# Kernel tuning notes

Hardware: AMD Instinct MI355X
Metric: run time of the kernel (lower is better)

## Reference

```python
import math
import jax, jax.numpy as jnp
import numpy as np
from jax import lax

B = 32; SEQ_LEN = 1024; PRED_LEN = 1024; ENC_IN = 7; MARK = 4; C_OUT = 7
D_MODEL = 128; D_INNER = 256; D_STATE = 16; D_CONV = 4; DT_RANK = 8; N_LAYER = 2


def setup_inputs() -> dict:
    key = jax.random.key(0)
    ks = jax.random.split(key, 16)
    f32 = jnp.float32
    inp = {}
    inp['x_enc'] = jax.random.normal(ks[0], (B, SEQ_LEN, ENC_IN), f32)
    inp['x_mark_enc'] = jax.random.uniform(ks[1], (B, SEQ_LEN, MARK), f32) - 0.5
    inp['x_dec'] = jax.random.normal(ks[2], (B, 512, ENC_IN), f32)
    inp['x_mark_dec'] = jax.random.uniform(ks[3], (B, 512, MARK), f32) - 0.5
    inp['token_W'] = jax.random.normal(ks[4], (D_MODEL, ENC_IN, 3), f32) * (1.0 / math.sqrt(3 * ENC_IN))
    inp['temporal_W'] = jax.random.normal(ks[5], (D_MODEL, MARK), f32) * 0.1
    inp['norm_w'] = jnp.ones((N_LAYER, D_MODEL), f32)
    inp['norm_b'] = jnp.zeros((N_LAYER, D_MODEL), f32)
    inp['in_proj_W'] = jax.random.normal(ks[6], (N_LAYER, 2 * D_INNER, D_MODEL), f32) * (1.0 / math.sqrt(D_MODEL))
    inp['conv_W'] = jax.random.normal(ks[7], (N_LAYER, D_INNER, D_CONV), f32) * 0.3
    inp['conv_b'] = jnp.zeros((N_LAYER, D_INNER), f32)
    inp['x_proj_W'] = jax.random.normal(ks[8], (N_LAYER, DT_RANK + 2 * D_STATE, D_INNER), f32) * (1.0 / math.sqrt(D_INNER))
    inp['dt_proj_W'] = jax.random.normal(ks[9], (N_LAYER, D_INNER, DT_RANK), f32) * (1.0 / math.sqrt(DT_RANK))
    inp['dt_proj_b'] = jax.random.normal(ks[10], (N_LAYER, D_INNER), f32) * 0.5 - 4.0  # softplus -> small dt, like mamba init
    inp['A_log'] = jnp.log(jnp.broadcast_to(jnp.arange(1, D_STATE + 1, dtype=f32), (N_LAYER, D_INNER, D_STATE)))
    inp['D_param'] = jnp.ones((N_LAYER, D_INNER), f32)
    inp['out_proj_W'] = jax.random.normal(ks[11], (N_LAYER, D_MODEL, D_INNER), f32) * (1.0 / math.sqrt(D_INNER))
    inp['normf_w'] = jnp.ones((D_MODEL,), f32)
    inp['normf_b'] = jnp.zeros((D_MODEL,), f32)
    inp['out_W'] = jax.random.normal(ks[12], (C_OUT, D_MODEL), f32) * (1.0 / math.sqrt(D_MODEL))
    return inp


def _layer_norm(x, w, b):
    mu = x.mean(-1, keepdims=True)
    var = ((x - mu) ** 2).mean(-1, keepdims=True)
    return (x - mu) * lax.rsqrt(var + 1e-5) * w + b


def _silu(x):
    return x * jax.nn.sigmoid(x)


def _pos_embedding(L, d):
    pos = jnp.arange(L, dtype=jnp.float32)[:, None]
    div = jnp.exp(jnp.arange(0, d, 2, dtype=jnp.float32) * (-math.log(10000.0) / d))
    pe = jnp.zeros((L, d), jnp.float32)
    pe = pe.at[:, 0::2].set(jnp.sin(pos * div))
    pe = pe.at[:, 1::2].set(jnp.cos(pos * div))
    return pe


def _embed(x_enc, x_mark_enc, token_W, temporal_W):
    # TokenEmbedding: Conv1d(enc_in->d_model, k=3, circular padding, no bias)
    xp = jnp.concatenate([x_enc[:, -1:], x_enc, x_enc[:, :1]], axis=1)  # circular pad by 1
    val = lax.conv_general_dilated(xp, token_W.transpose(2, 1, 0), (1,), 'VALID',
                                   dimension_numbers=('NWC', 'WIO', 'NWC'))
    temp = jnp.einsum('blf,df->bld', x_mark_enc, temporal_W)  # TimeFeatureEmbedding (no bias)
    return val + temp + _pos_embedding(x_enc.shape[1], D_MODEL)


def _mamba_mixer(x, in_W, cW, cb, xp_W, dtW, dtb, A_log_l, D_l, o_W):
    Bb, L, _ = x.shape
    xz = jnp.einsum('bld,ed->ble', x, in_W)  # [B,L,2*d_inner]
    xi, z = jnp.split(xz, 2, axis=-1)
    # causal depthwise conv1d (kernel d_conv)
    xpad = jnp.pad(xi, ((0, 0), (D_CONV - 1, 0), (0, 0)))
    kern = cW.T[:, None, :]  # [d_conv, 1, d_inner]
    u = lax.conv_general_dilated(xpad, kern, (1,), 'VALID', dimension_numbers=('NWC', 'WIO', 'NWC'),
                                 feature_group_count=D_INNER) + cb
    u = _silu(u)
    dbc = jnp.einsum('bld,ed->ble', u, xp_W)
    dt_r = dbc[..., :DT_RANK]
    Bm = dbc[..., DT_RANK:DT_RANK + D_STATE]
    Cm = dbc[..., DT_RANK + D_STATE:]
    dt = jax.nn.softplus(jnp.einsum('blr,dr->bld', dt_r, dtW) + dtb)  # [B,L,d_inner]
    A = -jnp.exp(A_log_l)  # [d_inner, d_state]

    def step(h, inp):
        dt_t, B_t, C_t, u_t = inp  # [B,d_inner], [B,d_state], [B,d_state], [B,d_inner]
        dA = jnp.exp(dt_t[..., None] * A)
        h = dA * h + dt_t[..., None] * B_t[:, None, :] * u_t[..., None]
        y = jnp.einsum('bds,bs->bd', h, C_t)
        return h, y

    h0 = jnp.zeros((Bb, D_INNER, D_STATE), x.dtype)
    _, ys = lax.scan(step, h0, (dt.transpose(1, 0, 2), Bm.transpose(1, 0, 2),
                                Cm.transpose(1, 0, 2), u.transpose(1, 0, 2)))
    y = ys.transpose(1, 0, 2) + u * D_l  # skip connection D*u
    y = y * _silu(z)
    return jnp.einsum('ble,de->bld', y, o_W)


def _mixer_model(x, norm_w, norm_b, in_proj_W, conv_W, conv_b, x_proj_W, dt_proj_W, dt_proj_b,
                 A_log, D_param, out_proj_W, normf_w, normf_b):
    hidden, residual = x, None
    for l in range(N_LAYER):
        residual = hidden if residual is None else hidden + residual
        hidden = _mamba_mixer(_layer_norm(residual, norm_w[l], norm_b[l]), in_proj_W[l], conv_W[l],
                              conv_b[l], x_proj_W[l], dt_proj_W[l], dt_proj_b[l], A_log[l],
                              D_param[l], out_proj_W[l])
    return _layer_norm(hidden + residual, normf_w, normf_b)


def reference(x_enc, x_mark_enc, x_dec, x_mark_dec, token_W, temporal_W, norm_w, norm_b,
              in_proj_W, conv_W, conv_b, x_proj_W, dt_proj_W, dt_proj_b, A_log, D_param,
              out_proj_W, normf_w, normf_b, out_W):
    h = _embed(x_enc, x_mark_enc, token_W, temporal_W)
    outs = []
    for _ in range((PRED_LEN - 1) // SEQ_LEN + 1):
        h = _mixer_model(h, norm_w, norm_b, in_proj_W, conv_W, conv_b, x_proj_W, dt_proj_W,
                         dt_proj_b, A_log, D_param, out_proj_W, normf_w, normf_b)
        outs.append(h)
    mamba_out = jnp.concatenate(outs, axis=1)[:, :PRED_LEN]
    return jnp.einsum('bld,cd->blc', mamba_out, out_W)
```

## Files before the change

kernel.cpp:

```cpp
#include <hip/hip_runtime.h>
#include <math.h>

#define B_  32
#define L_  1024
#define M_  (B_*L_)
#define DM  128
#define DI  256
#define DS  16
#define DC  4
#define DR  8
#define NL  2

typedef unsigned int  uint32;
typedef unsigned short ush;
typedef __attribute__((ext_vector_type(8))) short bf16x8;
typedef __attribute__((ext_vector_type(4))) float f32x4;

__device__ __forceinline__ float silu_f(float x) { return x / (1.f + expf(-x)); }
__device__ __forceinline__ float softplus_f(float x) {
    return fmaxf(x, 0.f) + log1pf(expf(-fabsf(x)));
}
__device__ __forceinline__ ush f2bf(float x) {
    union { float f; uint32 u; } v; v.f = x;
    uint32 lsb = (v.u >> 16) & 1u;
    v.u += 0x7fffu + lsb;
    return (ush)(v.u >> 16);
}
__device__ __forceinline__ void split2(float x, ush& h, ush& l) {
    h = f2bf(x);
    float fh = __uint_as_float(((uint32)h) << 16);
    l = f2bf(x - fh);
}
__device__ __forceinline__ uint32 pack_pair(float x) {
    ush h, l; split2(x, h, l);
    return (uint32)h | ((uint32)l << 16);
}
__device__ __forceinline__ float unpack_pair(uint32 v) {
    return __uint_as_float(v << 16) + __uint_as_float(v & 0xffff0000u);
}

__global__ __launch_bounds__(256) void cvt_pair_kernel(
        const float* __restrict__ src, ush* __restrict__ h, ush* __restrict__ l, int n) {
    int i = blockIdx.x * 256 + threadIdx.x;
    if (i < n) { ush hh, ll; split2(src[i], hh, ll); h[i] = hh; l[i] = ll; }
}

__global__ __launch_bounds__(256) void pe_kernel(float* __restrict__ pe) {
    int idx = blockIdx.x * 256 + threadIdx.x;
    int t = idx >> 6, i = idx & 63;
    float div = expf(-0.07195578415606394f * (float)(2 * i));
    float ang = (float)t * div;
    pe[t * 128 + 2 * i]     = sinf(ang);
    pe[t * 128 + 2 * i + 1] = cosf(ang);
}

__global__ __launch_bounds__(256) void embed_kernel(
        const float* __restrict__ x_enc, const float* __restrict__ x_mark,
        const float* __restrict__ tokW, const float* __restrict__ tempW,
        const float* __restrict__ pe, float* __restrict__ out) {
    int idx = blockIdx.x * 256 + threadIdx.x;
    int d = idx & 127;
    int m = idx >> 7;
    int b = m >> 10, t = m & 1023;
    const float* xb = x_enc + (size_t)b * L_ * 7;
    float acc = pe[t * 128 + d];
    #pragma unroll
    for (int w = 0; w < 3; ++w) {
        int tt = t + w - 1;
        tt = (tt < 0) ? (L_ - 1) : (tt >= L_ ? 0 : tt);
        const float* xr = xb + tt * 7;
        #pragma unroll
        for (int f = 0; f < 7; ++f) acc += xr[f] * tokW[(d * 7 + f) * 3 + w];
    }
    const float* mr = x_mark + (size_t)m * 4;
    #pragma unroll
    for (int f = 0; f < 4; ++f) acc += mr[f] * tempW[d * 4 + f];
    out[idx] = acc;
}

__global__ __launch_bounds__(256) void ln_kernel(
        const float* __restrict__ a, const float* __restrict__ b,
        const float* __restrict__ w, const float* __restrict__ bias,
        float* __restrict__ out_f32, ush* __restrict__ outh, ush* __restrict__ outl,
        float* __restrict__ out_res) {
    int wv = threadIdx.x >> 6, lane = threadIdx.x & 63;
    size_t m = (size_t)blockIdx.x * 4 + wv;
    size_t base = m * DM;
    float x0 = a[base + lane], x1 = a[base + lane + 64];
    if (b) { x0 += b[base + lane]; x1 += b[base + lane + 64]; }
    if (out_res) { out_res[base + lane] = x0; out_res[base + lane + 64] = x1; }
    float s = x0 + x1;
    #pragma unroll
    for (int o = 1; o < 64; o <<= 1) s += __shfl_xor(s, o, 64);
    float mu = s * (1.f / 128.f);
    float d0 = x0 - mu, d1 = x1 - mu;
    float v = d0 * d0 + d1 * d1;
    #pragma unroll
    for (int o = 1; o < 64; o <<= 1) v += __shfl_xor(v, o, 64);
    float inv = rsqrtf(v * (1.f / 128.f) + 1e-5f);
    float r0 = d0 * inv * w[lane]      + bias[lane];
    float r1 = d1 * inv * w[lane + 64] + bias[lane + 64];
    if (out_f32) {
        out_f32[base + lane] = r0; out_f32[base + lane + 64] = r1;
    } else {
        ush h, l;
        split2(r0, h, l); outh[base + lane] = h;      outl[base + lane] = l;
        split2(r1, h, l); outh[base + lane + 64] = h; outl[base + lane + 64] = l;
    }
}

__global__ __launch_bounds__(256) void gemm_inproj_mfma(
        const ush* __restrict__ Ah, const ush* __restrict__ Al,
        const ush* __restrict__ Wh, const ush* __restrict__ Wl,
        float* __restrict__ xiT, float* __restrict__ zsilT) {
    int bm = blockIdx.y * 128, bn = blockIdx.x * 128;
    int w = threadIdx.x >> 6, l = threadIdx.x & 63;
    int lm = l & 15, lk8 = (l >> 4) * 8;
    f32x4 acc[2][8];
    #pragma unroll
    for (int mi = 0; mi < 2; ++mi)
        #pragma unroll
        for (int ni = 0; ni < 8; ++ni) acc[mi][ni] = {0.f, 0.f, 0.f, 0.f};
    const ush* ah = Ah + (size_t)(bm + w * 32 + lm) * 128;
    const ush* al = Al + (size_t)(bm + w * 32 + lm) * 128;
    const ush* wh = Wh + (size_t)(bn + lm) * 128;
    const ush* wl = Wl + (size_t)(bn + lm) * 128;
    for (int k0 = 0; k0 < 128; k0 += 32) {
        bf16x8 aH[2], aL[2];
        #pragma unroll
        for (int mi = 0; mi < 2; ++mi) {
            aH[mi] = *(const bf16x8*)(ah + mi * 16 * 128 + k0 + lk8);
            aL[mi] = *(const bf16x8*)(al + mi * 16 * 128 + k0 + lk8);
        }
        #pragma unroll
        for (int ni = 0; ni < 8; ++ni) {
            bf16x8 wH = *(const bf16x8*)(wh + ni * 16 * 128 + k0 + lk8);
            bf16x8 wLo = *(const bf16x8*)(wl + ni * 16 * 128 + k0 + lk8);
            #pragma unroll
            for (int mi = 0; mi < 2; ++mi) {
                acc[mi][ni] = __builtin_amdgcn_mfma_f32_16x16x32_bf16(aL[mi], wH,  acc[mi][ni], 0, 0, 0);
                acc[mi][ni] = __builtin_amdgcn_mfma_f32_16x16x32_bf16(aH[mi], wLo, acc[mi][ni], 0, 0, 0);
                acc[mi][ni] = __builtin_amdgcn_mfma_f32_16x16x32_bf16(aH[mi], wH,  acc[mi][ni], 0, 0, 0);
            }
        }
    }
    int b = bm >> 10;
    int tl0 = (bm & 1023) + w * 32 + (l >> 4) * 4;
    #pragma unroll
    for (int ni = 0; ni < 8; ++ni) {
        int n = bn + ni * 16 + lm;
        #pragma unroll
        for (int mi = 0; mi < 2; ++mi) {
            int tl = tl0 + mi * 16;
            f32x4 v = acc[mi][ni];
            if (bn < 256) {
                *(f32x4*)(xiT + ((size_t)(b * 256 + n)) * 1024 + tl) = v;
            } else {
                f32x4 r;
                #pragma unroll
                for (int i = 0; i < 4; ++i) r[i] = silu_f(v[i]);
                *(f32x4*)(zsilT + ((size_t)(b * 256 + n - 256)) * 1024 + tl) = r;
            }
        }
    }
}

template<int NF, int KTOT>
__global__ __launch_bounds__(256) void gemm_at_mfma(
        const uint32* __restrict__ A32, const ush* __restrict__ Wh,
        const ush* __restrict__ Wl, int Nvalid,
        float* __restrict__ Cnm, float* __restrict__ Cmn) {
    __shared__ uint32 As[128][68];
    int bm = blockIdx.x * 128;
    int b = bm >> 10, tloc = bm & 1023;
    int tid = threadIdx.x;
    int w = tid >> 6, l = tid & 63;
    int lm = l & 15, lk8 = (l >> 4) * 8;
    f32x4 acc[2][NF];
    #pragma unroll
    for (int mi = 0; mi < 2; ++mi)
        #pragma unroll
        for (int ni = 0; ni < NF; ++ni) acc[mi][ni] = {0.f, 0.f, 0.f, 0.f};

    for (int k0 = 0; k0 < KTOT; k0 += 64) {
        __syncthreads();
        {
            int k = tid >> 2, mq = tid & 3;
            const uint32* src = A32 + ((size_t)(b * KTOT + k0 + k)) * 1024 + tloc + mq * 32;
            #pragma unroll
            for (int c = 0; c < 8; ++c) {
                uint4 v = *(const uint4*)(src + c * 4);
                As[mq * 32 + c * 4 + 0][k] = v.x;
                As[mq * 32 + c * 4 + 1][k] = v.y;
                As[mq * 32 + c * 4 + 2][k] = v.z;
                As[mq * 32 + c * 4 + 3][k] = v.w;
            }
        }
        __syncthreads();
        #pragma unroll
        for (int ks = 0; ks < 2; ++ks) {
            int kk = ks * 32 + lk8;
            bf16x8 aH[2], aL[2];
            #pragma unroll
            for (int mi = 0; mi < 2; ++mi) {
                int m = w * 32 + mi * 16 + lm;
                uint4 p0 = *(const uint4*)&As[m][kk];
                uint4 p1 = *(const uint4*)&As[m][kk + 4];
                uint32 u[8] = {p0.x, p0.y, p0.z, p0.w, p1.x, p1.y, p1.z, p1.w};
                bf16x8 h, lo;
                #pragma unroll
                for (int j = 0; j < 8; ++j) {
                    h[j]  = (short)(u[j] & 0xffffu);
                    lo[j] = (short)(u[j] >> 16);
                }
                aH[mi] = h; aL[mi] = lo;
            }
            #pragma unroll
            for (int ni = 0; ni < NF; ++ni) {
                int n = ni * 16 + lm;
                bf16x8 wH = {0,0,0,0,0,0,0,0}, wLo = {0,0,0,0,0,0,0,0};
                if (n < Nvalid) {
                    wH  = *(const bf16x8*)(Wh + (size_t)n * KTOT + k0 + ks * 32 + lk8);
                    wLo = *(const bf16x8*)(Wl + (size_t)n * KTOT + k0 + ks * 32 + lk8);
                }
                #pragma unroll
                for (int mi = 0; mi < 2; ++mi) {
                    acc[mi][ni] = __builtin_amdgcn_mfma_f32_16x16x32_bf16(aL[mi], wH,  acc[mi][ni], 0, 0, 0);
                    acc[mi][ni] = __builtin_amdgcn_mfma_f32_16x16x32_bf16(aH[mi], wLo, acc[mi][ni], 0, 0, 0);
                    acc[mi][ni] = __builtin_amdgcn_mfma_f32_16x16x32_bf16(aH[mi], wH,  acc[mi][ni], 0, 0, 0);
                }
            }
        }
    }
    int m0 = w * 32 + (l >> 4) * 4;
    #pragma unroll
    for (int ni = 0; ni < NF; ++ni) {
        int n = ni * 16 + lm;
        #pragma unroll
        for (int mi = 0; mi < 2; ++mi) {
            f32x4 v = acc[mi][ni];
            int mg = bm + m0 + mi * 16;
            if (Cnm) {
                if (n < Nvalid) *(f32x4*)(Cnm + (size_t)n * M_ + mg) = v;
            } else {
                #pragma unroll
                for (int r = 0; r < 4; ++r)
                    Cmn[(size_t)(mg + r) * Nvalid + n] = v[r];
            }
        }
    }
}

__global__ __launch_bounds__(256) void conv_T_kernel(
        const float* __restrict__ xiT, const float* __restrict__ cw,
        const float* __restrict__ cb, uint32* __restrict__ uT32) {
    int wv = threadIdx.x >> 6, lane = threadIdx.x & 63;
    int rid = blockIdx.x * 4 + wv;
    int d = rid & 255;
    const float* src = xiT + (size_t)rid * 1024;
    int t0 = lane * 16;
    float x[20];
    {
        float4 p = (lane > 0) ? *(const float4*)(src + t0 - 4)
                              : make_float4(0.f, 0.f, 0.f, 0.f);
        *(float4*)&x[0] = p;
        #pragma unroll
        for (int c = 0; c < 4; ++c)
            *(float4*)&x[4 + c * 4] = *(const float4*)(src + t0 + c * 4);
    }
    float4 w4 = ((const float4*)cw)[d];
    float bias = cb[d];
    uint32* dst = uT32 + (size_t)rid * 1024 + t0;
    #pragma unroll
    for (int c = 0; c < 4; ++c) {
        uint4 o;
        uint32 ov[4];
        #pragma unroll
        for (int i = 0; i < 4; ++i) {
            int k = c * 4 + i;
            float acc = bias + x[k + 1] * w4.x + x[k + 2] * w4.y
                             + x[k + 3] * w4.z + x[k + 4] * w4.w;
            ov[i] = pack_pair(silu_f(acc));
        }
        o.x = ov[0]; o.y = ov[1]; o.z = ov[2]; o.w = ov[3];
        *(uint4*)(dst + c * 4) = o;
    }
}

__global__ __launch_bounds__(256) void dtT_kernel(
        const float* __restrict__ dbcT, const float* __restrict__ dtW,
        const float* __restrict__ dtb, float* __restrict__ dtT) {
    int n = threadIdx.x;
    int m0 = blockIdx.x * 64;
    int b = m0 >> 10, t0 = m0 & 1023;
    float wk[8];
    *(float4*)&wk[0] = ((const float4*)dtW)[n * 2];
    *(float4*)&wk[4] = ((const float4*)dtW)[n * 2 + 1];
    float bias = dtb[n];
    float* dst = dtT + ((size_t)(b * 256 + n)) * 1024 + t0;
    for (int r4 = 0; r4 < 64; r4 += 4) {
        float col[8][4];
        #pragma unroll
        for (int k = 0; k < 8; ++k)
            *(float4*)col[k] = *(const float4*)(dbcT + (size_t)k * M_ + m0 + r4);
        float o[4];
        #pragma unroll
        for (int i = 0; i < 4; ++i) {
            float a = bias;
            #pragma unroll
            for (int k = 0; k < 8; ++k) a += col[k][i] * wk[k];
            o[i] = softplus_f(a);
        }
        *(float4*)(dst + r4) = make_float4(o[0], o[1], o[2], o[3]);
    }
}

__global__ __launch_bounds__(256) void scan5_kernel(
        const float* __restrict__ dtT, const uint32* __restrict__ uT32,
        const float* __restrict__ dbcT, const float* __restrict__ A_log,
        const float* __restrict__ zsilT, const float* __restrict__ Dp,
        uint32* __restrict__ yT32) {
    int wv = threadIdx.x >> 6, lane = threadIdx.x & 63;
    int wid = blockIdx.x * 4 + wv;
    int b = wid >> 8, d = wid & 255;
    size_t base = (size_t)wid * 1024 + lane * 16;

    float dt[16], du[16], y[16], pcA[16], pcB[16];
    {
        const float4* p = (const float4*)(dtT + base);
        const uint4*  q = (const uint4*)(uT32 + base);
        #pragma unroll
        for (int c = 0; c < 4; ++c) {
            float4 dv = p[c]; uint4 uv = q[c];
            dt[c * 4 + 0] = dv.x; dt[c * 4 + 1] = dv.y; dt[c * 4 + 2] = dv.z; dt[c * 4 + 3] = dv.w;
            du[c * 4 + 0] = dv.x * unpack_pair(uv.x);
            du[c * 4 + 1] = dv.y * unpack_pair(uv.y);
            du[c * 4 + 2] = dv.z * unpack_pair(uv.z);
            du[c * 4 + 3] = dv.w * unpack_pair(uv.w);
        }
        #pragma unroll
        for (int i = 0; i < 16; ++i) y[i] = 0.f;
    }
    const float* Bb = dbcT + (size_t)8  * M_ + (size_t)b * 1024 + lane * 16;
    const float* Cb = dbcT + (size_t)24 * M_ + (size_t)b * 1024 + lane * 16;
    const float* Arow = A_log + d * 16;

    for (int p = 0; p < 8; ++p) {
        int s0 = 2 * p, s1 = 2 * p + 1;
        float4 B0[4], B1[4], C0[4], C1[4];
        #pragma unroll
        for (int c = 0; c < 4; ++c) {
            B0[c] = *(const float4*)(Bb + (size_t)s0 * M_ + c * 4);
            B1[c] = *(const float4*)(Bb + (size_t)s1 * M_ + c * 4);
            C0[c] = *(const float4*)(Cb + (size_t)s0 * M_ + c * 4);
            C1[c] = *(const float4*)(Cb + (size_t)s1 * M_ + c * 4);
        }
        float A2a = -expf(Arow[s0]) * 1.4426950408889634f;
        float A2b = -expf(Arow[s1]) * 1.4426950408889634f;
        float h0 = 0.f, P0 = 1.f, h1 = 0.f, P1 = 1.f;
        #pragma unroll
        for (int c = 0; c < 4; ++c) {
            float Bv0[4] = {B0[c].x, B0[c].y, B0[c].z, B0[c].w};
            float Cv0[4] = {C0[c].x, C0[c].y, C0[c].z, C0[c].w};
            float Bv1[4] = {B1[c].x, B1[c].y, B1[c].z, B1[c].w};
            float Cv1[4] = {C1[c].x, C1[c].y, C1[c].z, C1[c].w};
            #pragma unroll
            for (int i = 0; i < 4; ++i) {
                int ii = c * 4 + i;
                float a0 = __builtin_amdgcn_exp2f(dt[ii] * A2a);
                float a1 = __builtin_amdgcn_exp2f(dt[ii] * A2b);
                h0 = a0 * h0 + du[ii] * Bv0[i];  P0 *= a0;
                h1 = a1 * h1 + du[ii] * Bv1[i];  P1 *= a1;
                y[ii] += h0 * Cv0[i] + h1 * Cv1[i];
                pcA[ii] = P0 * Cv0[i];
                pcB[ii] = P1 * Cv1[i];
            }
        }
        float Aag0 = P0, E0 = h0, Aag1 = P1, E1 = h1;
        #pragma unroll
        for (int dlt = 1; dlt < 64; dlt <<= 1) {
            float Au0 = __shfl_up(Aag0, dlt, 64), Eu0 = __shfl_up(E0, dlt, 64);
            float Au1 = __shfl_up(Aag1, dlt, 64), Eu1 = __shfl_up(E1, dlt, 64);
            if (lane >= dlt) {
                E0 = Aag0 * Eu0 + E0;  Aag0 *= Au0;
                E1 = Aag1 * Eu1 + E1;  Aag1 *= Au1;
            }
        }
        float car0 = __shfl_up(E0, 1, 64), car1 = __shfl_up(E1, 1, 64);
        if (lane == 0) { car0 = 0.f; car1 = 0.f; }
        #pragma unroll
        for (int i = 0; i < 16; ++i) y[i] += car0 * pcA[i] + car1 * pcB[i];
    }

    float Dv = Dp[d];
    const float4* qz = (const float4*)(zsilT + base);
    uint32* dst = yT32 + base;
    #pragma unroll
    for (int c = 0; c < 4; ++c) {
        float4 zv = qz[c];
        float za[4] = {zv.x, zv.y, zv.z, zv.w};
        uint32 ov[4];
        #pragma unroll
        for (int i = 0; i < 4; ++i) {
            int ii = c * 4 + i;
            float u = (dt[ii] > 0.f) ? du[ii] * __builtin_amdgcn_rcpf(dt[ii]) : 0.f;
            ov[i] = pack_pair((y[ii] + u * Dv) * za[i]);
        }
        uint4 o; o.x = ov[0]; o.y = ov[1]; o.z = ov[2]; o.w = ov[3];
        *(uint4*)(dst + c * 4) = o;
    }
}

__global__ __launch_bounds__(256) void outproj_kernel(
        const float* __restrict__ x, const float* __restrict__ W,
        float* __restrict__ out) {
    int wv = threadIdx.x >> 6, lane = threadIdx.x & 63;
    size_t m = (size_t)blockIdx.x * 4 + wv;
    float x0 = x[m * 128 + lane], x1 = x[m * 128 + lane + 64];
    #pragma unroll
    for (int c = 0; c < 7; ++c) {
        float p = x0 * W[c * 128 + lane] + x1 * W[c * 128 + lane + 64];
        #pragma unroll
        for (int o = 1; o < 64; o <<= 1) p += __shfl_xor(p, o, 64);
        if (lane == 0) out[m * 7 + c] = p;
    }
}

extern "C" void kernel_launch(void* const* d_in, const int* in_sizes, int n_in,
                              void* d_out, int out_size, void* d_ws, size_t ws_size,
                              hipStream_t stream) {
    const float* x_enc  = (const float*)d_in[0];
    const float* x_mark = (const float*)d_in[1];
    const float* tokW   = (const float*)d_in[4];
    const float* tempW  = (const float*)d_in[5];
    const float* norm_w = (const float*)d_in[6];
    const float* norm_b = (const float*)d_in[7];
    const float* inW    = (const float*)d_in[8];
    const float* convW  = (const float*)d_in[9];
    const float* convB  = (const float*)d_in[10];
    const float* xpW    = (const float*)d_in[11];
    const float* dtW    = (const float*)d_in[12];
    const float* dtbp   = (const float*)d_in[13];
    const float* A_log  = (const float*)d_in[14];
    const float* Dp     = (const float*)d_in[15];
    const float* outW   = (const float*)d_in[16];
    const float* nfw    = (const float*)d_in[17];
    const float* nfb    = (const float*)d_in[18];
    const float* finW   = (const float*)d_in[19];
    float* out = (float*)d_out;

    float* ws = (float*)d_ws;
    size_t o = 0;
    float*  hidden   = ws + o; o += (size_t)M_ * DM;
    float*  residual = ws + o; o += (size_t)M_ * DM;
    float*  xlnF     = ws + o; o += (size_t)M_ * DM;
    float*  xiT      = ws + o; o += (size_t)M_ * DI;
    float*  zsilT    = ws + o; o += (size_t)M_ * DI;
    uint32* uT32     = (uint32*)(ws + o); o += (size_t)M_ * DI;
    float*  dbcT     = ws + o; o += (size_t)M_ * 40;
    float*  dtT      = ws + o; o += (size_t)M_ * DI;
    uint32* yT32     = (uint32*)(ws + o); o += (size_t)M_ * DI;
    ush* inWh  = (ush*)(ws + o); o += (size_t)NL * 512 * DM / 2;
    ush* inWl  = (ush*)(ws + o); o += (size_t)NL * 512 * DM / 2;
    ush* xpWh  = (ush*)(ws + o); o += (size_t)NL * 40 * DI / 2;
    ush* xpWl  = (ush*)(ws + o); o += (size_t)NL * 40 * DI / 2;
    ush* outWh = (ush*)(ws + o); o += (size_t)NL * DM * DI / 2;
    ush* outWl = (ush*)(ws + o); o += (size_t)NL * DM * DI / 2;
    ush* xlnh = (ush*)xlnF;
    ush* xlnl = xlnh + (size_t)M_ * DM;
    float* pe = dbcT;

    dim3 blk(256);
    pe_kernel<<<1024 * 64 / 256, blk, 0, stream>>>(pe);
    embed_kernel<<<M_ * DM / 256, blk, 0, stream>>>(x_enc, x_mark, tokW, tempW, pe, hidden);
    {
        int n1 = NL * 512 * DM, n2 = NL * 40 * DI, n3 = NL * DM * DI;
        cvt_pair_kernel<<<(n1 + 255) / 256, blk, 0, stream>>>(inW,  inWh,  inWl,  n1);
        cvt_pair_kernel<<<(n2 + 255) / 256, blk, 0, stream>>>(xpW,  xpWh,  xpWl,  n2);
        cvt_pair_kernel<<<(n3 + 255) / 256, blk, 0, stream>>>(outW, outWh, outWl, n3);
    }

    for (int l = 0; l < NL; ++l) {
        ln_kernel<<<M_ / 4, blk, 0, stream>>>(hidden, l ? residual : nullptr,
                                              norm_w + l * DM, norm_b + l * DM,
                                              nullptr, xlnh, xlnl, residual);
        gemm_inproj_mfma<<<dim3(4, M_ / 128), blk, 0, stream>>>(
            xlnh, xlnl, inWh + (size_t)l * 512 * DM, inWl + (size_t)l * 512 * DM,
            xiT, zsilT);
        conv_T_kernel<<<B_ * DI / 4, blk, 0, stream>>>(xiT, convW + l * DI * DC,
                                                       convB + l * DI, uT32);
        gemm_at_mfma<3, 256><<<M_ / 128, blk, 0, stream>>>(
            uT32, xpWh + (size_t)l * 40 * DI, xpWl + (size_t)l * 40 * DI,
            40, dbcT, nullptr);
        dtT_kernel<<<M_ / 64, blk, 0, stream>>>(dbcT, dtW + l * DI * DR,
                                                dtbp + l * DI, dtT);
        scan5_kernel<<<B_ * DI / 4, blk, 0, stream>>>(dtT, uT32, dbcT,
                                                      A_log + l * DI * DS, zsilT,
                                                      Dp + l * DI, yT32);
        gemm_at_mfma<8, 256><<<M_ / 128, blk, 0, stream>>>(
            yT32, outWh + (size_t)l * DM * DI, outWl + (size_t)l * DM * DI,
            128, nullptr, hidden);
    }

    ln_kernel<<<M_ / 4, blk, 0, stream>>>(hidden, residual, nfw, nfb,
                                          xlnF, nullptr, nullptr, nullptr);
    outproj_kernel<<<M_ / 4, blk, 0, stream>>>(xlnF, finW, out);
}
```

Measured before the change: 629.4 us.

## Fuse dt projection into scan kernel and final layernorm into output projection

The dt projection plus softplus is now computed inside the scan kernel from the dbc rows, so the separate dtT kernel and its M×256 float intermediate buffer are gone. The final layernorm is fused with the 7-channel output projection, which removes one full-size write and read of the normalized hidden state and one kernel launch. In exchange, the scan does extra loads of the 8 dt-rank rows and extra FMAs and softplus per element, repeated across the 256 channels of each batch.

```diff
diff --git a/kernel.cpp b/kernel.cpp
--- a/kernel.cpp
+++ b/kernel.cpp
@@ -81,14 +81,14 @@
 __global__ __launch_bounds__(256) void ln_kernel(
         const float* __restrict__ a, const float* __restrict__ b,
         const float* __restrict__ w, const float* __restrict__ bias,
-        float* __restrict__ out_f32, ush* __restrict__ outh, ush* __restrict__ outl,
+        ush* __restrict__ outh, ush* __restrict__ outl,
         float* __restrict__ out_res) {
     int wv = threadIdx.x >> 6, lane = threadIdx.x & 63;
     size_t m = (size_t)blockIdx.x * 4 + wv;
     size_t base = m * DM;
     float x0 = a[base + lane], x1 = a[base + lane + 64];
     if (b) { x0 += b[base + lane]; x1 += b[base + lane + 64]; }
-    if (out_res) { out_res[base + lane] = x0; out_res[base + lane + 64] = x1; }
+    out_res[base + lane] = x0; out_res[base + lane + 64] = x1;
     float s = x0 + x1;
     #pragma unroll
     for (int o = 1; o < 64; o <<= 1) s += __shfl_xor(s, o, 64);
@@ -100,12 +100,37 @@
     float inv = rsqrtf(v * (1.f / 128.f) + 1e-5f);
     float r0 = d0 * inv * w[lane]      + bias[lane];
     float r1 = d1 * inv * w[lane + 64] + bias[lane + 64];
-    if (out_f32) {
-        out_f32[base + lane] = r0; out_f32[base + lane + 64] = r1;
-    } else {
-        ush h, l;
-        split2(r0, h, l); outh[base + lane] = h;      outl[base + lane] = l;
-        split2(r1, h, l); outh[base + lane + 64] = h; outl[base + lane + 64] = l;
+    ush h, l;
+    split2(r0, h, l); outh[base + lane] = h;      outl[base + lane] = l;
+    split2(r1, h, l); outh[base + lane + 64] = h; outl[base + lane + 64] = l;
+}
+
+__global__ __launch_bounds__(256) void ln_out_kernel(
+        const float* __restrict__ a, const float* __restrict__ b,
+        const float* __restrict__ w, const float* __restrict__ bias,
+        const float* __restrict__ finW, float* __restrict__ out) {
+    int wv = threadIdx.x >> 6, lane = threadIdx.x & 63;
+    size_t m = (size_t)blockIdx.x * 4 + wv;
+    size_t base = m * DM;
+    float x0 = a[base + lane] + b[base + lane];
+    float x1 = a[base + lane + 64] + b[base + lane + 64];
+    float s = x0 + x1;
+    #pragma unroll
+    for (int o = 1; o < 64; o <<= 1) s += __shfl_xor(s, o, 64);
+    float mu = s * (1.f / 128.f);
+    float d0 = x0 - mu, d1 = x1 - mu;
+    float v = d0 * d0 + d1 * d1;
+    #pragma unroll
+    for (int o = 1; o < 64; o <<= 1) v += __shfl_xor(v, o, 64);
+    float inv = rsqrtf(v * (1.f / 128.f) + 1e-5f);
+    float r0 = d0 * inv * w[lane]      + bias[lane];
+    float r1 = d1 * inv * w[lane + 64] + bias[lane + 64];
+    #pragma unroll
+    for (int c = 0; c < 7; ++c) {
+        float p = r0 * finW[c * 128 + lane] + r1 * finW[c * 128 + lane + 64];
+        #pragma unroll
+        for (int o = 1; o < 64; o <<= 1) p += __shfl_xor(p, o, 64);
+        if (lane == 0) out[m * 7 + c] = p;
     }
 }
 
@@ -287,62 +312,48 @@
     }
 }
 
-__global__ __launch_bounds__(256) void dtT_kernel(
-        const float* __restrict__ dbcT, const float* __restrict__ dtW,
-        const float* __restrict__ dtb, float* __restrict__ dtT) {
-    int n = threadIdx.x;
-    int m0 = blockIdx.x * 64;
-    int b = m0 >> 10, t0 = m0 & 1023;
-    float wk[8];
-    *(float4*)&wk[0] = ((const float4*)dtW)[n * 2];
-    *(float4*)&wk[4] = ((const float4*)dtW)[n * 2 + 1];
-    float bias = dtb[n];
-    float* dst = dtT + ((size_t)(b * 256 + n)) * 1024 + t0;
-    for (int r4 = 0; r4 < 64; r4 += 4) {
-        float col[8][4];
-        #pragma unroll
-        for (int k = 0; k < 8; ++k)
-            *(float4*)col[k] = *(const float4*)(dbcT + (size_t)k * M_ + m0 + r4);
-        float o[4];
-        #pragma unroll
-        for (int i = 0; i < 4; ++i) {
-            float a = bias;
-            #pragma unroll
-            for (int k = 0; k < 8; ++k) a += col[k][i] * wk[k];
-            o[i] = softplus_f(a);
-        }
-        *(float4*)(dst + r4) = make_float4(o[0], o[1], o[2], o[3]);
-    }
-}
-
-__global__ __launch_bounds__(256) void scan5_kernel(
-        const float* __restrict__ dtT, const uint32* __restrict__ uT32,
-        const float* __restrict__ dbcT, const float* __restrict__ A_log,
-        const float* __restrict__ zsilT, const float* __restrict__ Dp,
-        uint32* __restrict__ yT32) {
+__global__ __launch_bounds__(256) void scan6_kernel(
+        const uint32* __restrict__ uT32, const float* __restrict__ dbcT,
+        const float* __restrict__ A_log, const float* __restrict__ zsilT,
+        const float* __restrict__ Dp, const float* __restrict__ dtW,
+        const float* __restrict__ dtb, uint32* __restrict__ yT32) {
     int wv = threadIdx.x >> 6, lane = threadIdx.x & 63;
     int wid = blockIdx.x * 4 + wv;
     int b = wid >> 8, d = wid & 255;
     size_t base = (size_t)wid * 1024 + lane * 16;
+    size_t m0 = (size_t)b * 1024 + lane * 16;
+
+    float wk[8];
+    *(float4*)&wk[0] = ((const float4*)dtW)[d * 2];
+    *(float4*)&wk[4] = ((const float4*)dtW)[d * 2 + 1];
+    float bias = dtb[d];
 
     float dt[16], du[16], y[16], pcA[16], pcB[16];
     {
-        const float4* p = (const float4*)(dtT + base);
-        const uint4*  q = (const uint4*)(uT32 + base);
+        const uint4* q = (const uint4*)(uT32 + base);
         #pragma unroll
         for (int c = 0; c < 4; ++c) {
-            float4 dv = p[c]; uint4 uv = q[c];
-            dt[c * 4 + 0] = dv.x; dt[c * 4 + 1] = dv.y; dt[c * 4 + 2] = dv.z; dt[c * 4 + 3] = dv.w;
-            du[c * 4 + 0] = dv.x * unpack_pair(uv.x);
-            du[c * 4 + 1] = dv.y * unpack_pair(uv.y);
-            du[c * 4 + 2] = dv.z * unpack_pair(uv.z);
-            du[c * 4 + 3] = dv.w * unpack_pair(uv.w);
+            float col[8][4];
+            #pragma unroll
+            for (int k = 0; k < 8; ++k)
+                *(float4*)col[k] = *(const float4*)(dbcT + (size_t)k * M_ + m0 + c * 4);
+            uint4 uv = q[c];
+            uint32 ua[4] = {uv.x, uv.y, uv.z, uv.w};
+            #pragma unroll
+            for (int i = 0; i < 4; ++i) {
+                float a = bias;
+                #pragma unroll
+                for (int k = 0; k < 8; ++k) a = fmaf(col[k][i], wk[k], a);
+                float dtv = softplus_f(a);
+                dt[c * 4 + i] = dtv;
+                du[c * 4 + i] = dtv * unpack_pair(ua[i]);
+            }
         }
         #pragma unroll
         for (int i = 0; i < 16; ++i) y[i] = 0.f;
     }
-    const float* Bb = dbcT + (size_t)8  * M_ + (size_t)b * 1024 + lane * 16;
-    const float* Cb = dbcT + (size_t)24 * M_ + (size_t)b * 1024 + lane * 16;
+    const float* Bb = dbcT + (size_t)8  * M_ + m0;
+    const float* Cb = dbcT + (size_t)24 * M_ + m0;
     const float* Arow = A_log + d * 16;
 
     for (int p = 0; p < 8; ++p) {
@@ -408,21 +419,6 @@
         }
         uint4 o; o.x = ov[0]; o.y = ov[1]; o.z = ov[2]; o.w = ov[3];
         *(uint4*)(dst + c * 4) = o;
-    }
-}
-
-__global__ __launch_bounds__(256) void outproj_kernel(
-        const float* __restrict__ x, const float* __restrict__ W,
-        float* __restrict__ out) {
-    int wv = threadIdx.x >> 6, lane = threadIdx.x & 63;
-    size_t m = (size_t)blockIdx.x * 4 + wv;
-    float x0 = x[m * 128 + lane], x1 = x[m * 128 + lane + 64];
-    #pragma unroll
-    for (int c = 0; c < 7; ++c) {
-        float p = x0 * W[c * 128 + lane] + x1 * W[c * 128 + lane + 64];
-        #pragma unroll
-        for (int o = 1; o < 64; o <<= 1) p += __shfl_xor(p, o, 64);
-        if (lane == 0) out[m * 7 + c] = p;
     }
 }
 
@@ -453,12 +449,11 @@
     size_t o = 0;
     float*  hidden   = ws + o; o += (size_t)M_ * DM;
     float*  residual = ws + o; o += (size_t)M_ * DM;
-    float*  xlnF     = ws + o; o += (size_t)M_ * DM;
+    float*  xlnP     = ws + o; o += (size_t)M_ * DM;
     float*  xiT      = ws + o; o += (size_t)M_ * DI;
     float*  zsilT    = ws + o; o += (size_t)M_ * DI;
     uint32* uT32     = (uint32*)(ws + o); o += (size_t)M_ * DI;
     float*  dbcT     = ws + o; o += (size_t)M_ * 40;
-    float*  dtT      = ws + o; o += (size_t)M_ * DI;
     uint32* yT32     = (uint32*)(ws + o); o += (size_t)M_ * DI;
     ush* inWh  = (ush*)(ws + o); o += (size_t)NL * 512 * DM / 2;
     ush* inWl  = (ush*)(ws + o); o += (size_t)NL * 512 * DM / 2;
@@ -466,7 +461,7 @@
     ush* xpWl  = (ush*)(ws + o); o += (size_t)NL * 40 * DI / 2;
     ush* outWh = (ush*)(ws + o); o += (size_t)NL * DM * DI / 2;
     ush* outWl = (ush*)(ws + o); o += (size_t)NL * DM * DI / 2;
-    ush* xlnh = (ush*)xlnF;
+    ush* xlnh = (ush*)xlnP;
     ush* xlnl = xlnh + (size_t)M_ * DM;
     float* pe = dbcT;
 
@@ -483,7 +478,7 @@
     for (int l = 0; l < NL; ++l) {
         ln_kernel<<<M_ / 4, blk, 0, stream>>>(hidden, l ? residual : nullptr,
                                               norm_w + l * DM, norm_b + l * DM,
-                                              nullptr, xlnh, xlnl, residual);
+                                              xlnh, xlnl, residual);
         gemm_inproj_mfma<<<dim3(4, M_ / 128), blk, 0, stream>>>(
             xlnh, xlnl, inWh + (size_t)l * 512 * DM, inWl + (size_t)l * 512 * DM,
             xiT, zsilT);
@@ -492,17 +487,15 @@
         gemm_at_mfma<3, 256><<<M_ / 128, blk, 0, stream>>>(
             uT32, xpWh + (size_t)l * 40 * DI, xpWl + (size_t)l * 40 * DI,
             40, dbcT, nullptr);
-        dtT_kernel<<<M_ / 64, blk, 0, stream>>>(dbcT, dtW + l * DI * DR,
-                                                dtbp + l * DI, dtT);
-        scan5_kernel<<<B_ * DI / 4, blk, 0, stream>>>(dtT, uT32, dbcT,
+        scan6_kernel<<<B_ * DI / 4, blk, 0, stream>>>(uT32, dbcT,
                                                       A_log + l * DI * DS, zsilT,
-                                                      Dp + l * DI, yT32);
+                                                      Dp + l * DI,
+                                                      dtW + (size_t)l * DI * DR,
+                                                      dtbp + l * DI, yT32);
         gemm_at_mfma<8, 256><<<M_ / 128, blk, 0, stream>>>(
             yT32, outWh + (size_t)l * DM * DI, outWl + (size_t)l * DM * DI,
             128, nullptr, hidden);
     }
 
-    ln_kernel<<<M_ / 4, blk, 0, stream>>>(hidden, residual, nfw, nfb,
-                                          xlnF, nullptr, nullptr, nullptr);
-    outproj_kernel<<<M_ / 4, blk, 0, stream>>>(xlnF, finW, out);
-}
+    ln_out_kernel<<<M_ / 4, blk, 0, stream>>>(hidden, residual, nfw, nfb, finW, out);
+}
```

Result: faster. 600.9 us (-4.5%).

## Split scan sequence across two waves, prefetch B/C, fuse final LN with output projection

Applied to the files above, without the earlier changes.

The selective scan now assigns each (batch, channel) sequence to two wavefronts, each handling 512 timesteps with 8 per lane. The first half's carry is passed through shared memory with a block barrier, which doubles the number of waves for better latency hiding and fewer registers per lane. B/C state loads are software-prefetched one state pair ahead, and the p loop is fully unrolled. Separately, the final layer norm is fused with the 7-channel output projection, which drops a full f32 intermediate write and read; the cost is an extra __syncthreads per state pair in the scan.

```diff
diff --git a/kernel.cpp b/kernel.cpp
--- a/kernel.cpp
+++ b/kernel.cpp
@@ -81,14 +81,14 @@
 __global__ __launch_bounds__(256) void ln_kernel(
         const float* __restrict__ a, const float* __restrict__ b,
         const float* __restrict__ w, const float* __restrict__ bias,
-        float* __restrict__ out_f32, ush* __restrict__ outh, ush* __restrict__ outl,
+        ush* __restrict__ outh, ush* __restrict__ outl,
         float* __restrict__ out_res) {
     int wv = threadIdx.x >> 6, lane = threadIdx.x & 63;
     size_t m = (size_t)blockIdx.x * 4 + wv;
     size_t base = m * DM;
     float x0 = a[base + lane], x1 = a[base + lane + 64];
     if (b) { x0 += b[base + lane]; x1 += b[base + lane + 64]; }
-    if (out_res) { out_res[base + lane] = x0; out_res[base + lane + 64] = x1; }
+    out_res[base + lane] = x0; out_res[base + lane + 64] = x1;
     float s = x0 + x1;
     #pragma unroll
     for (int o = 1; o < 64; o <<= 1) s += __shfl_xor(s, o, 64);
@@ -100,12 +100,37 @@
     float inv = rsqrtf(v * (1.f / 128.f) + 1e-5f);
     float r0 = d0 * inv * w[lane]      + bias[lane];
     float r1 = d1 * inv * w[lane + 64] + bias[lane + 64];
-    if (out_f32) {
-        out_f32[base + lane] = r0; out_f32[base + lane + 64] = r1;
-    } else {
-        ush h, l;
-        split2(r0, h, l); outh[base + lane] = h;      outl[base + lane] = l;
-        split2(r1, h, l); outh[base + lane + 64] = h; outl[base + lane + 64] = l;
+    ush h, l;
+    split2(r0, h, l); outh[base + lane] = h;      outl[base + lane] = l;
+    split2(r1, h, l); outh[base + lane + 64] = h; outl[base + lane + 64] = l;
+}
+
+__global__ __launch_bounds__(256) void ln_out_kernel(
+        const float* __restrict__ a, const float* __restrict__ b,
+        const float* __restrict__ w, const float* __restrict__ bias,
+        const float* __restrict__ finW, float* __restrict__ out) {
+    int wv = threadIdx.x >> 6, lane = threadIdx.x & 63;
+    size_t m = (size_t)blockIdx.x * 4 + wv;
+    size_t base = m * DM;
+    float x0 = a[base + lane] + b[base + lane];
+    float x1 = a[base + lane + 64] + b[base + lane + 64];
+    float s = x0 + x1;
+    #pragma unroll
+    for (int o = 1; o < 64; o <<= 1) s += __shfl_xor(s, o, 64);
+    float mu = s * (1.f / 128.f);
+    float d0 = x0 - mu, d1 = x1 - mu;
+    float v = d0 * d0 + d1 * d1;
+    #pragma unroll
+    for (int o = 1; o < 64; o <<= 1) v += __shfl_xor(v, o, 64);
+    float inv = rsqrtf(v * (1.f / 128.f) + 1e-5f);
+    float r0 = d0 * inv * w[lane]      + bias[lane];
+    float r1 = d1 * inv * w[lane + 64] + bias[lane + 64];
+    #pragma unroll
+    for (int c = 0; c < 7; ++c) {
+        float p = r0 * finW[c * 128 + lane] + r1 * finW[c * 128 + lane + 64];
+        #pragma unroll
+        for (int o = 1; o < 64; o <<= 1) p += __shfl_xor(p, o, 64);
+        if (lane == 0) out[m * 7 + c] = p;
     }
 }
 
@@ -315,22 +340,25 @@
     }
 }
 
-__global__ __launch_bounds__(256) void scan5_kernel(
+__global__ __launch_bounds__(256) void scan7_kernel(
         const float* __restrict__ dtT, const uint32* __restrict__ uT32,
         const float* __restrict__ dbcT, const float* __restrict__ A_log,
         const float* __restrict__ zsilT, const float* __restrict__ Dp,
         uint32* __restrict__ yT32) {
-    int wv = threadIdx.x >> 6, lane = threadIdx.x & 63;
-    int wid = blockIdx.x * 4 + wv;
+    __shared__ float sh[2][2][2];
+    int w = threadIdx.x >> 6, lane = threadIdx.x & 63;
+    int half = w & 1, rl = w >> 1;
+    int wid = blockIdx.x * 2 + rl;
     int b = wid >> 8, d = wid & 255;
-    size_t base = (size_t)wid * 1024 + lane * 16;
-
-    float dt[16], du[16], y[16], pcA[16], pcB[16];
+    size_t base = (size_t)wid * 1024 + half * 512 + (size_t)lane * 8;
+    size_t mrow = (size_t)b * 1024 + half * 512 + (size_t)lane * 8;
+
+    float dt[8], du[8], y[8], pcA[8], pcB[8];
     {
         const float4* p = (const float4*)(dtT + base);
         const uint4*  q = (const uint4*)(uT32 + base);
         #pragma unroll
-        for (int c = 0; c < 4; ++c) {
+        for (int c = 0; c < 2; ++c) {
             float4 dv = p[c]; uint4 uv = q[c];
             dt[c * 4 + 0] = dv.x; dt[c * 4 + 1] = dv.y; dt[c * 4 + 2] = dv.z; dt[c * 4 + 3] = dv.w;
             du[c * 4 + 0] = dv.x * unpack_pair(uv.x);
@@ -339,27 +367,41 @@
             du[c * 4 + 3] = dv.w * unpack_pair(uv.w);
         }
         #pragma unroll
-        for (int i = 0; i < 16; ++i) y[i] = 0.f;
-    }
-    const float* Bb = dbcT + (size_t)8  * M_ + (size_t)b * 1024 + lane * 16;
-    const float* Cb = dbcT + (size_t)24 * M_ + (size_t)b * 1024 + lane * 16;
+        for (int i = 0; i < 8; ++i) y[i] = 0.f;
+    }
+    const float* Bb = dbcT + (size_t)8  * M_ + mrow;
+    const float* Cb = dbcT + (size_t)24 * M_ + mrow;
     const float* Arow = A_log + d * 16;
 
+    float4 nB0[2], nB1[2], nC0[2], nC1[2];
+    #pragma unroll
+    for (int c = 0; c < 2; ++c) {
+        nB0[c] = *(const float4*)(Bb + c * 4);
+        nB1[c] = *(const float4*)(Bb + (size_t)M_ + c * 4);
+        nC0[c] = *(const float4*)(Cb + c * 4);
+        nC1[c] = *(const float4*)(Cb + (size_t)M_ + c * 4);
+    }
+
+    #pragma unroll
     for (int p = 0; p < 8; ++p) {
-        int s0 = 2 * p, s1 = 2 * p + 1;
-        float4 B0[4], B1[4], C0[4], C1[4];
-        #pragma unroll
-        for (int c = 0; c < 4; ++c) {
-            B0[c] = *(const float4*)(Bb + (size_t)s0 * M_ + c * 4);
-            B1[c] = *(const float4*)(Bb + (size_t)s1 * M_ + c * 4);
-            C0[c] = *(const float4*)(Cb + (size_t)s0 * M_ + c * 4);
-            C1[c] = *(const float4*)(Cb + (size_t)s1 * M_ + c * 4);
-        }
-        float A2a = -expf(Arow[s0]) * 1.4426950408889634f;
-        float A2b = -expf(Arow[s1]) * 1.4426950408889634f;
+        float4 B0[2], B1[2], C0[2], C1[2];
+        #pragma unroll
+        for (int c = 0; c < 2; ++c) { B0[c] = nB0[c]; B1[c] = nB1[c]; C0[c] = nC0[c]; C1[c] = nC1[c]; }
+        if (p < 7) {
+            size_t s0 = (size_t)(2 * p + 2) * M_, s1 = (size_t)(2 * p + 3) * M_;
+            #pragma unroll
+            for (int c = 0; c < 2; ++c) {
+                nB0[c] = *(const float4*)(Bb + s0 + c * 4);
+                nB1[c] = *(const float4*)(Bb + s1 + c * 4);
+                nC0[c] = *(const float4*)(Cb + s0 + c * 4);
+                nC1[c] = *(const float4*)(Cb + s1 + c * 4);
+            }
+        }
+        float A2a = -expf(Arow[2 * p])     * 1.4426950408889634f;
+        float A2b = -expf(Arow[2 * p + 1]) * 1.4426950408889634f;
         float h0 = 0.f, P0 = 1.f, h1 = 0.f, P1 = 1.f;
         #pragma unroll
-        for (int c = 0; c < 4; ++c) {
+        for (int c = 0; c < 2; ++c) {
             float Bv0[4] = {B0[c].x, B0[c].y, B0[c].z, B0[c].w};
             float Cv0[4] = {C0[c].x, C0[c].y, C0[c].z, C0[c].w};
             float Bv1[4] = {B1[c].x, B1[c].y, B1[c].z, B1[c].w};
@@ -386,17 +428,24 @@
                 E1 = Aag1 * Eu1 + E1;  Aag1 *= Au1;
             }
         }
-        float car0 = __shfl_up(E0, 1, 64), car1 = __shfl_up(E1, 1, 64);
-        if (lane == 0) { car0 = 0.f; car1 = 0.f; }
-        #pragma unroll
-        for (int i = 0; i < 16; ++i) y[i] += car0 * pcA[i] + car1 * pcB[i];
+        if (half == 0 && lane == 63) { sh[p & 1][rl][0] = E0; sh[p & 1][rl][1] = E1; }
+        __syncthreads();
+        float SA0 = half ? sh[p & 1][rl][0] : 0.f;
+        float SA1 = half ? sh[p & 1][rl][1] : 0.f;
+        float Eu0 = __shfl_up(E0, 1, 64), Au0 = __shfl_up(Aag0, 1, 64);
+        float Eu1 = __shfl_up(E1, 1, 64), Au1 = __shfl_up(Aag1, 1, 64);
+        if (lane == 0) { Eu0 = 0.f; Au0 = 1.f; Eu1 = 0.f; Au1 = 1.f; }
+        float car0 = Eu0 + Au0 * SA0;
+        float car1 = Eu1 + Au1 * SA1;
+        #pragma unroll
+        for (int i = 0; i < 8; ++i) y[i] += car0 * pcA[i] + car1 * pcB[i];
     }
 
     float Dv = Dp[d];
     const float4* qz = (const float4*)(zsilT + base);
     uint32* dst = yT32 + base;
     #pragma unroll
-    for (int c = 0; c < 4; ++c) {
+    for (int c = 0; c < 2; ++c) {
         float4 zv = qz[c];
         float za[4] = {zv.x, zv.y, zv.z, zv.w};
         uint32 ov[4];
@@ -408,21 +457,6 @@
         }
         uint4 o; o.x = ov[0]; o.y = ov[1]; o.z = ov[2]; o.w = ov[3];
         *(uint4*)(dst + c * 4) = o;
-    }
-}
-
-__global__ __launch_bounds__(256) void outproj_kernel(
-        const float* __restrict__ x, const float* __restrict__ W,
-        float* __restrict__ out) {
-    int wv = threadIdx.x >> 6, lane = threadIdx.x & 63;
-    size_t m = (size_t)blockIdx.x * 4 + wv;
-    float x0 = x[m * 128 + lane], x1 = x[m * 128 + lane + 64];
-    #pragma unroll
-    for (int c = 0; c < 7; ++c) {
-        float p = x0 * W[c * 128 + lane] + x1 * W[c * 128 + lane + 64];
-        #pragma unroll
-        for (int o = 1; o < 64; o <<= 1) p += __shfl_xor(p, o, 64);
-        if (lane == 0) out[m * 7 + c] = p;
     }
 }
 
@@ -453,7 +487,7 @@
     size_t o = 0;
     float*  hidden   = ws + o; o += (size_t)M_ * DM;
     float*  residual = ws + o; o += (size_t)M_ * DM;
-    float*  xlnF     = ws + o; o += (size_t)M_ * DM;
+    float*  xlnP     = ws + o; o += (size_t)M_ * DM;
     float*  xiT      = ws + o; o += (size_t)M_ * DI;
     float*  zsilT    = ws + o; o += (size_t)M_ * DI;
     uint32* uT32     = (uint32*)(ws + o); o += (size_t)M_ * DI;
@@ -466,7 +500,7 @@
     ush* xpWl  = (ush*)(ws + o); o += (size_t)NL * 40 * DI / 2;
     ush* outWh = (ush*)(ws + o); o += (size_t)NL * DM * DI / 2;
     ush* outWl = (ush*)(ws + o); o += (size_t)NL * DM * DI / 2;
-    ush* xlnh = (ush*)xlnF;
+    ush* xlnh = (ush*)xlnP;
     ush* xlnl = xlnh + (size_t)M_ * DM;
     float* pe = dbcT;
 
@@ -483,7 +517,7 @@
     for (int l = 0; l < NL; ++l) {
         ln_kernel<<<M_ / 4, blk, 0, stream>>>(hidden, l ? residual : nullptr,
                                               norm_w + l * DM, norm_b + l * DM,
-                                              nullptr, xlnh, xlnl, residual);
+                                              xlnh, xlnl, residual);
         gemm_inproj_mfma<<<dim3(4, M_ / 128), blk, 0, stream>>>(
             xlnh, xlnl, inWh + (size_t)l * 512 * DM, inWl + (size_t)l * 512 * DM,
             xiT, zsilT);
@@ -494,7 +528,7 @@
             40, dbcT, nullptr);
         dtT_kernel<<<M_ / 64, blk, 0, stream>>>(dbcT, dtW + l * DI * DR,
                                                 dtbp + l * DI, dtT);
-        scan5_kernel<<<B_ * DI / 4, blk, 0, stream>>>(dtT, uT32, dbcT,
+        scan7_kernel<<<B_ * DI / 2, blk, 0, stream>>>(dtT, uT32, dbcT,
                                                       A_log + l * DI * DS, zsilT,
                                                       Dp + l * DI, yT32);
         gemm_at_mfma<8, 256><<<M_ / 128, blk, 0, stream>>>(
@@ -502,7 +536,5 @@
             128, nullptr, hidden);
     }
 
-    ln_kernel<<<M_ / 4, blk, 0, stream>>>(hidden, residual, nfw, nfb,
-                                          xlnF, nullptr, nullptr, nullptr);
-    outproj_kernel<<<M_ / 4, blk, 0, stream>>>(xlnF, finW, out);
-}
+    ln_out_kernel<<<M_ / 4, blk, 0, stream>>>(hidden, residual, nfw, nfb, finW, out);
+}
```

Result: slower. 888.1 us (+41.1%).
